# Performance work log

Measured on AMD Instinct MI355X. Metric: run time of the kernel, lower is better.

The kernel has to match this reference:

```python
import jax, jax.numpy as jnp
import numpy as np

N = 100000      # points
M = 12500       # cluster centers
E0 = 1600000    # point-level edges
E1 = 400000     # cluster-level edges
F_IN = 4        # raw point feature dim (e.g. intensity + extras)
D = 64          # hidden feature width
N_CLASSES = 8


def setup_inputs() -> dict:
    key = jax.random.key(0)
    ks = jax.random.split(key, 20)
    s = 0.05
    d = {}
    d["features"] = jax.random.normal(ks[0], (N, F_IN), jnp.float32)
    d["points"] = jax.random.normal(ks[1], (N, 3), jnp.float32)
    d["cluster_centers"] = jax.random.normal(ks[2], (M, 3), jnp.float32)
    d["l0_edges"] = jax.random.randint(ks[3], (E0, 2), 0, N)
    d["l1_edges"] = jax.random.randint(ks[4], (E1, 2), 0, M)
    d["labels"] = jax.random.randint(ks[5], (N,), 0, M)
    # Feature_extract MLP
    d["W_fe"] = s * jax.random.normal(ks[6], (F_IN + 3, D), jnp.float32)
    d["b_fe"] = jnp.zeros((D,), jnp.float32)
    # 4 Mini_GNN layers (layer2, layer2_1, layer6, layer6_1), stacked
    d["mini_We"] = s * jax.random.normal(ks[7], (4, D + 3, D), jnp.float32)
    d["mini_be"] = jnp.zeros((4, D), jnp.float32)
    d["mini_Wu"] = s * jax.random.normal(ks[8], (4, D, D), jnp.float32)
    d["mini_bu"] = jnp.zeros((4, D), jnp.float32)
    # Mini_to_Large
    d["W_m1"] = s * jax.random.normal(ks[9], (D + 3, D), jnp.float32)
    d["b_m1"] = jnp.zeros((D,), jnp.float32)
    d["W_m2"] = s * jax.random.normal(ks[10], (D, D), jnp.float32)
    d["b_m2"] = jnp.zeros((D,), jnp.float32)
    # 2 GNN layers on cluster graph (layer4, layer4_1), stacked
    d["gnn_We"] = s * jax.random.normal(ks[11], (2, D + 3, D), jnp.float32)
    d["gnn_be"] = jnp.zeros((2, D), jnp.float32)
    d["gnn_Wu"] = s * jax.random.normal(ks[12], (2, D, D), jnp.float32)
    d["gnn_bu"] = jnp.zeros((2, D), jnp.float32)
    # Large_to_Mini
    d["W_l"] = s * jax.random.normal(ks[13], (D + 3, D), jnp.float32)
    d["b_l"] = jnp.zeros((D,), jnp.float32)
    # Classifier
    d["W_c"] = s * jax.random.normal(ks[14], (D, N_CLASSES), jnp.float32)
    d["b_c"] = jnp.zeros((N_CLASSES,), jnp.float32)
    return d


def _gnn_layer(feat, pos, edges, We, be, Wu, bu, n_nodes):
    """PointGNN-style layer: gather -> edge MLP -> scatter max -> update MLP -> residual."""
    src, dst = edges[:, 0], edges[:, 1]
    e_in = jnp.concatenate([pos[src] - pos[dst], feat[src]], axis=-1)  # [E, 3+D]
    h = jax.nn.relu(e_in @ We + be)                                     # [E, D]
    agg = jax.ops.segment_max(h, dst, num_segments=n_nodes)            # [n, D]
    agg = jnp.where(jnp.isneginf(agg), 0.0, agg)  # nodes with no in-edges -> 0
    return jax.nn.relu(agg @ Wu + bu) + feat


def reference(features, points, cluster_centers, l0_edges, l1_edges, labels,
              W_fe, b_fe, mini_We, mini_be, mini_Wu, mini_bu,
              W_m1, b_m1, W_m2, b_m2, gnn_We, gnn_be, gnn_Wu, gnn_bu,
              W_l, b_l, W_c, b_c):
    rel = points - cluster_centers[labels]  # [N, 3] point pos relative to its cluster
    # layer1: Feature_extract
    f1 = jax.nn.relu(jnp.concatenate([features, rel], -1) @ W_fe + b_fe)
    # layer2 / layer2_1: Mini_GNN (scatter max) on point graph
    f2 = _gnn_layer(f1, points, l0_edges, mini_We[0], mini_be[0], mini_Wu[0], mini_bu[0], N)
    f2_1 = _gnn_layer(f2, points, l0_edges, mini_We[1], mini_be[1], mini_Wu[1], mini_bu[1], N)
    # layer3: Mini_to_Large (scatter sum by labels)
    h = jax.nn.relu(jnp.concatenate([f2_1, rel], -1) @ W_m1 + b_m1)
    c = jax.ops.segment_sum(h, labels, num_segments=M)  # [M, D]
    f3 = jax.nn.relu(c @ W_m2 + b_m2)
    # layer4 / layer4_1: GNN (scatter max) on cluster graph
    f4 = _gnn_layer(f3, cluster_centers, l1_edges, gnn_We[0], gnn_be[0], gnn_Wu[0], gnn_bu[0], M)
    f4_1 = _gnn_layer(f4, cluster_centers, l1_edges, gnn_We[1], gnn_be[1], gnn_Wu[1], gnn_bu[1], M)
    # layer5: Large_to_Mini (gather by labels)
    f5 = jax.nn.relu(jnp.concatenate([f4_1[labels], rel], -1) @ W_l + b_l)
    # layer6 / layer6_1 with residual skips per call()
    f6 = _gnn_layer(f5, points, l0_edges, mini_We[2], mini_be[2], mini_Wu[2], mini_bu[2], N)
    f6 = f6 + f2_1
    f6_1 = _gnn_layer(f6, points, l0_edges, mini_We[3], mini_be[3], mini_Wu[3], mini_bu[3], N)
    final = f6_1 + f2
    return final @ W_c + b_c  # [N, N_CLASSES] per-point logits
```

## Files before the change

### kernel.cpp

```cpp
#include <hip/hip_runtime.h>

#define N_PTS   100000
#define M_CL    12500
#define E0_N    1600000
#define E1_N    400000

#define NB      256
#define BIN_CAP 32
#define RANGE0  391
#define RANGE1  49
#define BCAP0   8192
#define BCAP1   2048
#define BCAPL   1024

#define LSTR    72

typedef unsigned short ushortT;
typedef short  short8 __attribute__((ext_vector_type(8)));
typedef float  v4f    __attribute__((ext_vector_type(4)));
typedef _Float16 h2   __attribute__((ext_vector_type(2)));
typedef unsigned u4v  __attribute__((ext_vector_type(4)));

__device__ inline ushortT f2bf(float x){
  union{float f; unsigned u;} v; v.f = x;
  unsigned r = v.u + 0x7fffu + ((v.u >> 16) & 1u);
  return (ushortT)(r >> 16);
}
__device__ inline float bf2f(ushortT h){
  union{unsigned u; float f;} v; v.u = ((unsigned)h) << 16;
  return v.f;
}
__device__ inline ushortT f2h(float x){
  union{_Float16 h; ushortT u;} v; v.h = (_Float16)x;
  return v.u;
}
__device__ inline float h2f(ushortT u){
  union{ushortT u; _Float16 h;} v; v.u = u;
  return (float)v.h;
}
__device__ inline h2 pkmax(h2 a, h2 b){ return __builtin_elementwise_max(a, b); }
__device__ inline h2 u2h(unsigned u){ union{unsigned u; h2 h;} v{u}; return v.h; }


struct WSrc { const float* p[16]; };

__global__ __launch_bounds__(256) void k_init_wprep(WSrc s, ushortT* __restrict__ wt, ushortT* __restrict__ wtc,
                                                    int* c0, int* c1, int* cL){
  int blk = blockIdx.x;
  if (blk == 0){
    int t = threadIdx.x;
    c0[t] = t*BCAP0; c1[t] = t*BCAP1; cL[t] = t*BCAPL;
    return;
  }
  int slot = blk - 1;
  if (slot < 15){
    const float* src = s.p[slot];
    ushortT* dst = wt + slot*4096;
    for (int e=threadIdx.x; e<4096; e+=256){
      int nn = e>>6, kk = e&63;
      dst[e] = f2bf(src[kk*64+nn]);
    }
  } else {
    const float* src = s.p[15];
    for (int e=threadIdx.x; e<1024; e+=256){
      int nn = e>>6, kk = e&63;
      wtc[e] = (nn<8) ? f2bf(src[kk*8+nn]) : (ushortT)0;
    }
  }
}


template<int RANGE, bool LAB>
__device__ void bin_seg(const int* __restrict__ edges, int E,
                        int* __restrict__ bcur, unsigned* __restrict__ tmp,
                        int bid, int nblk,
                        unsigned* stage, int* scnt, int* sbase){
  int tid = threadIdx.x;
  int nchunks = (E + 2047) / 2048;
  for (int c = bid; c < nchunks; c += nblk){
    int base = c*2048;
    scnt[tid] = 0;
    __syncthreads();
    #pragma unroll
    for (int r=0;r<8;++r){
      int e = base + r*256 + tid;
      if (e < E){
        int s, d;
        if (LAB){ s = e; d = edges[e]; }
        else    { s = edges[2*e]; d = edges[2*e+1]; }
        int bk = d / RANGE;
        unsigned packed = ((unsigned)s << 11) | (unsigned)(d - bk*RANGE);
        int pos = atomicAdd(&scnt[bk], 1);
        if (pos < BIN_CAP) stage[bk*BIN_CAP+pos] = packed;
        else tmp[atomicAdd(&bcur[bk],1)] = packed;
      }
    }
    __syncthreads();
    {
      int nfl = scnt[tid]; if (nfl > BIN_CAP) nfl = BIN_CAP;
      sbase[tid] = atomicAdd(&bcur[tid], nfl);
    }
    __syncthreads();
    int wv = tid >> 6, ln = tid & 63;
    for (int bb=0; bb<32; ++bb){
      int bk = wv*64 + bb*2 + (ln>>5);
      int ent = ln & 31;
      int nf = scnt[bk]; if (nf > BIN_CAP) nf = BIN_CAP;
      if (ent < nf) tmp[sbase[bk]+ent] = stage[bk*BIN_CAP+ent];
    }
    __syncthreads();
  }
}

__global__ __launch_bounds__(256) void k_bin_all(const int* __restrict__ l0e, const int* __restrict__ l1e,
                                                 const int* __restrict__ labels,
                                                 int* bc0, int* bc1, int* bcL,
                                                 unsigned* t0, unsigned* t1, unsigned* tL){
  __shared__ unsigned stage[NB*BIN_CAP];
  __shared__ int scnt[NB];
  __shared__ int sbase[NB];
  int b = blockIdx.x;
  if (b < 256)      bin_seg<RANGE0,false>(l0e, E0_N, bc0, t0, b, 256, stage, scnt, sbase);
  else if (b < 452) bin_seg<RANGE1,false>(l1e, E1_N, bc1, t1, b-256, 196, stage, scnt, sbase);
  else              bin_seg<RANGE1,true >(labels, N_PTS, bcL, tL, b-452, 49, stage, scnt, sbase);
}

__global__ void k_scan_all(const int* c0, int* bb0, int* e0,
                           const int* c1, int* bb1, int* e1,
                           const int* cL, int* bbL, int* eL){
  const int* cur; int* bb; int* offe; int BC;
  if (blockIdx.x == 0){ cur=c0; bb=bb0; offe=e0; BC=BCAP0; }
  else if (blockIdx.x == 1){ cur=c1; bb=bb1; offe=e1; BC=BCAP1; }
  else { cur=cL; bb=bbL; offe=eL; BC=BCAPL; }
  int lane = threadIdx.x & 63;
  int base = lane*4;
  int v0 = cur[base+0] - (base+0)*BC;
  int v1 = cur[base+1] - (base+1)*BC;
  int v2 = cur[base+2] - (base+2)*BC;
  int v3 = cur[base+3] - (base+3)*BC;
  int psum = v0+v1+v2+v3, sc = psum;
  #pragma unroll
  for (int st=1; st<64; st<<=1){
    int x = __shfl_up(sc, st, 64);
    if (lane >= st) sc += x;
  }
  int ex = sc - psum;
  bb[base+0] = ex;
  bb[base+1] = ex + v0;
  bb[base+2] = ex + v0 + v1;
  bb[base+3] = ex + v0 + v1 + v2;
  if (lane == 63) *offe = sc;
}

template<int RANGE, int BCAP, int K>
__device__ void csr_build_seg(const unsigned* __restrict__ tmp, const int* __restrict__ bcur,
                              const int* __restrict__ bb, int n,
                              int* __restrict__ offs, int* __restrict__ csr,
                              int b, int* hist, int* part){
  int tid = threadIdx.x;
  int dlo = b*RANGE;
  int range = n - dlo; if (range > RANGE) range = RANGE; if (range < 0) range = 0;
  int cnt = bcur[b] - b*BCAP;
  for (int t=tid; t<RANGE; t+=256) hist[t] = 0;
  __syncthreads();
  const unsigned* sl = tmp + (size_t)b*BCAP;
  for (int j=tid; j<cnt; j+=256) atomicAdd(&hist[sl[j] & 2047u], 1);
  __syncthreads();
  int s = 0; int loc[K];
  #pragma unroll
  for (int kk=0; kk<K; ++kk){
    int idx = tid*K + kk;
    int v = (idx < RANGE) ? hist[idx] : 0;
    loc[kk] = s; s += v;
  }
  part[tid] = s; __syncthreads();
  int own = s;
  for (int st=1; st<256; st<<=1){
    int x = (tid >= st) ? part[tid-st] : 0;
    __syncthreads();
    part[tid] += x;
    __syncthreads();
  }
  int ebase = part[tid] - own;
  int gb = bb[b];
  __syncthreads();
  #pragma unroll
  for (int kk=0; kk<K; ++kk){
    int idx = tid*K + kk;
    if (idx < RANGE){
      int ex = ebase + loc[kk];
      if (idx < range) offs[dlo+idx] = gb + ex;
      hist[idx] = ex;
    }
  }
  __syncthreads();
  for (int j=tid; j<cnt; j+=256){
    unsigned p = sl[j];
    int pos = atomicAdd(&hist[p & 2047u], 1);
    csr[gb + pos] = (int)(p >> 11);
  }
}

__global__ __launch_bounds__(256) void k_build_all(
    const unsigned* t0, const int* bc0, const int* bb0, int* offs0, int* csr0,
    const unsigned* t1, const int* bc1, const int* bb1, int* offs1, int* csr1,
    const unsigned* tL, const int* bcL, const int* bbL, int* offsL, int* csrL){
  __shared__ int hist[RANGE0];
  __shared__ int part[256];
  int b = blockIdx.x;
  if (b < 256)      csr_build_seg<RANGE0,BCAP0,2>(t0, bc0, bb0, N_PTS, offs0, csr0, b, hist, part);
  else if (b < 512) csr_build_seg<RANGE1,BCAP1,1>(t1, bc1, bb1, M_CL, offs1, csr1, b-256, hist, part);
  else              csr_build_seg<RANGE1,BCAPL,1>(tL, bcL, bbL, M_CL, offsL, csrL, b-512, hist, part);
}


__global__ __launch_bounds__(256) void k_f1g(const float* __restrict__ features, const float* __restrict__ points,
                                             const float* __restrict__ centers, const int* __restrict__ labels,
                                             const float* __restrict__ W, const float* __restrict__ b,
                                             const ushortT* __restrict__ Wt2, const float* __restrict__ bias2,
                                             const float* __restrict__ Wr2,
                                             float* __restrict__ rel, ushortT* __restrict__ f1b,
                                             ushortT* __restrict__ gout, int n, int ntiles){
  __shared__ ushortT lds[4*16*LSTR];
  int tid = threadIdx.x;
  int lane = tid & 63, wslot = tid >> 6;
  int quad = lane >> 4, l15 = lane & 15;
  int gw = (blockIdx.x*256 + tid) >> 6;
  int nw = (gridDim.x*256) >> 6;
  float Wf0=W[0*64+lane], Wf1=W[1*64+lane], Wf2=W[2*64+lane], Wf3=W[3*64+lane];
  float wr0=W[4*64+lane], wr1=W[5*64+lane], wr2=W[6*64+lane];
  float bias=b[lane];
  short8 s0_0 = *(const short8*)(Wt2 + ( 0 + l15)*64 +  0 + quad*8);
  short8 s0_1 = *(const short8*)(Wt2 + ( 0 + l15)*64 + 32 + quad*8);
  short8 s1_0 = *(const short8*)(Wt2 + (16 + l15)*64 +  0 + quad*8);
  short8 s1_1 = *(const short8*)(Wt2 + (16 + l15)*64 + 32 + quad*8);
  short8 s2_0 = *(const short8*)(Wt2 + (32 + l15)*64 +  0 + quad*8);
  short8 s2_1 = *(const short8*)(Wt2 + (32 + l15)*64 + 32 + quad*8);
  short8 s3_0 = *(const short8*)(Wt2 + (48 + l15)*64 +  0 + quad*8);
  short8 s3_1 = *(const short8*)(Wt2 + (48 + l15)*64 + 32 + quad*8);
  float eb0 = bias2[l15], eb1 = bias2[16+l15], eb2 = bias2[32+l15], eb3 = bias2[48+l15];
  float e0c0=Wr2[0*64+l15], e0c1=Wr2[0*64+16+l15], e0c2=Wr2[0*64+32+l15], e0c3=Wr2[0*64+48+l15];
  float e1c0=Wr2[1*64+l15], e1c1=Wr2[1*64+16+l15], e1c2=Wr2[1*64+32+l15], e1c3=Wr2[1*64+48+l15];
  float e2c0=Wr2[2*64+l15], e2c1=Wr2[2*64+16+l15], e2c2=Wr2[2*64+32+l15], e2c3=Wr2[2*64+48+l15];

  for (int t=gw; t<ntiles; t+=nw){
    int i0 = t*16;
    for (int r=0;r<16;++r){
      int row = i0 + r;
      bool ok = row < n;
      int rr = ok ? row : n-1;
      int lb = labels[rr];
      float rx = points[rr*3+0]-centers[lb*3+0];
      float ry = points[rr*3+1]-centers[lb*3+1];
      float rz = points[rr*3+2]-centers[lb*3+2];
      float acc = bias + wr0*rx + wr1*ry + wr2*rz;
      acc += features[rr*4+0]*Wf0 + features[rr*4+1]*Wf1;
      acc += features[rr*4+2]*Wf2 + features[rr*4+3]*Wf3;
      acc = fmaxf(acc, 0.f);
      ushortT ab = f2bf(acc);
      if (ok){
        f1b[(size_t)row*64+lane] = ab;
        if (lane==0){ rel[row*3+0]=rx; rel[row*3+1]=ry; rel[row*3+2]=rz; }
      }
      lds[wslot*(16*LSTR) + r*LSTR + lane] = ab;
    }
    __builtin_amdgcn_wave_barrier();
    const ushortT* lp = lds + wslot*(16*LSTR) + l15*LSTR + quad*8;
    short8 sa0 = *(const short8*)(lp);
    short8 sa1 = *(const short8*)(lp + 32);
    __builtin_amdgcn_wave_barrier();
    v4f ec0 = {0.f,0.f,0.f,0.f}, ec1 = ec0, ec2 = ec0, ec3 = ec0;
    ec0 = __builtin_amdgcn_mfma_f32_16x16x32_bf16(sa0, s0_0, ec0, 0,0,0);
    ec1 = __builtin_amdgcn_mfma_f32_16x16x32_bf16(sa0, s1_0, ec1, 0,0,0);
    ec2 = __builtin_amdgcn_mfma_f32_16x16x32_bf16(sa0, s2_0, ec2, 0,0,0);
    ec3 = __builtin_amdgcn_mfma_f32_16x16x32_bf16(sa0, s3_0, ec3, 0,0,0);
    ec0 = __builtin_amdgcn_mfma_f32_16x16x32_bf16(sa1, s0_1, ec0, 0,0,0);
    ec1 = __builtin_amdgcn_mfma_f32_16x16x32_bf16(sa1, s1_1, ec1, 0,0,0);
    ec2 = __builtin_amdgcn_mfma_f32_16x16x32_bf16(sa1, s2_1, ec2, 0,0,0);
    ec3 = __builtin_amdgcn_mfma_f32_16x16x32_bf16(sa1, s3_1, ec3, 0,0,0);
    #pragma unroll
    for (int r=0;r<4;++r){
      int row = i0 + quad*4 + r;
      if (row < n){
        float vx=points[row*3+0], vy=points[row*3+1], vz=points[row*3+2];
        float g0 = ec0[r] + eb0 + vx*e0c0 + vy*e1c0 + vz*e2c0;
        float g1 = ec1[r] + eb1 + vx*e0c1 + vy*e1c1 + vz*e2c1;
        float g2 = ec2[r] + eb2 + vx*e0c2 + vy*e1c2 + vz*e2c2;
        float g3 = ec3[r] + eb3 + vx*e0c3 + vy*e1c3 + vz*e2c3;
        size_t base = (size_t)row*64 + l15;
        gout[base] = f2h(g0); gout[base+16] = f2h(g1); gout[base+32] = f2h(g2); gout[base+48] = f2h(g3);
      }
    }
  }
}


template<bool RELU, int NRES, bool USEREL, bool GATHER, bool OUT16, bool F16O, int EMODE, bool ERELU>
__global__ __launch_bounds__(256) void k_gemm(
    const ushortT* __restrict__ A, const ushortT* __restrict__ Wt,
    const float* __restrict__ bias, const float* __restrict__ Wr,
    const float* __restrict__ rel, const int* __restrict__ gidx,
    const ushortT* __restrict__ r1, const ushortT* __restrict__ r2,
    ushortT* __restrict__ out16,
    const ushortT* __restrict__ Wt2, const float* __restrict__ bias2,
    const float* __restrict__ Wr2, const float* __restrict__ vec2,
    void* __restrict__ eout,
    int n, int ntiles)
{
  constexpr int LDSZ = (EMODE>0) ? 4*16*LSTR : 4;
  __shared__ ushortT lds[LDSZ];
  int tid = threadIdx.x;
  int lane = tid & 63, wslot = tid >> 6;
  int quad = lane >> 4, l15 = lane & 15;
  int gw = (blockIdx.x*256 + tid) >> 6;
  int nw = (gridDim.x*256) >> 6;

  short8 bfr0_0 = *(const short8*)(Wt + ( 0 + l15)*64 +  0 + quad*8);
  short8 bfr0_1 = *(const short8*)(Wt + ( 0 + l15)*64 + 32 + quad*8);
  short8 bfr1_0 = *(const short8*)(Wt + (16 + l15)*64 +  0 + quad*8);
  short8 bfr1_1 = *(const short8*)(Wt + (16 + l15)*64 + 32 + quad*8);
  short8 bfr2_0 = *(const short8*)(Wt + (32 + l15)*64 +  0 + quad*8);
  short8 bfr2_1 = *(const short8*)(Wt + (32 + l15)*64 + 32 + quad*8);
  short8 bfr3_0 = *(const short8*)(Wt + (48 + l15)*64 +  0 + quad*8);
  short8 bfr3_1 = *(const short8*)(Wt + (48 + l15)*64 + 32 + quad*8);
  float bs0 = bias[ 0 + l15], bs1 = bias[16 + l15];
  float bs2 = bias[32 + l15], bs3 = bias[48 + l15];
  float w0c0=0,w0c1=0,w0c2=0,w0c3=0, w1c0=0,w1c1=0,w1c2=0,w1c3=0, w2c0=0,w2c1=0,w2c2=0,w2c3=0;
  if (USEREL){
    w0c0=Wr[0*64+l15]; w0c1=Wr[0*64+16+l15]; w0c2=Wr[0*64+32+l15]; w0c3=Wr[0*64+48+l15];
    w1c0=Wr[1*64+l15]; w1c1=Wr[1*64+16+l15]; w1c2=Wr[1*64+32+l15]; w1c3=Wr[1*64+48+l15];
    w2c0=Wr[2*64+l15]; w2c1=Wr[2*64+16+l15]; w2c2=Wr[2*64+32+l15]; w2c3=Wr[2*64+48+l15];
  }

  short8 s0_0{}, s0_1{}, s1_0{}, s1_1{}, s2_0{}, s2_1{}, s3_0{}, s3_1{};
  float eb0=0, eb1=0, eb2=0, eb3=0;
  float e0c0=0,e0c1=0,e0c2=0,e0c3=0, e1c0=0,e1c1=0,e1c2=0,e1c3=0, e2c0=0,e2c1=0,e2c2=0,e2c3=0;
  float ebias_c = 0.f;
  if (EMODE == 1){
    s0_0 = *(const short8*)(Wt2 + ( 0 + l15)*64 +  0 + quad*8);
    s0_1 = *(const short8*)(Wt2 + ( 0 + l15)*64 + 32 + quad*8);
    s1_0 = *(const short8*)(Wt2 + (16 + l15)*64 +  0 + quad*8);
    s1_1 = *(const short8*)(Wt2 + (16 + l15)*64 + 32 + quad*8);
    s2_0 = *(const short8*)(Wt2 + (32 + l15)*64 +  0 + quad*8);
    s2_1 = *(const short8*)(Wt2 + (32 + l15)*64 + 32 + quad*8);
    s3_0 = *(const short8*)(Wt2 + (48 + l15)*64 +  0 + quad*8);
    s3_1 = *(const short8*)(Wt2 + (48 + l15)*64 + 32 + quad*8);
    eb0 = bias2[l15]; eb1 = bias2[16+l15]; eb2 = bias2[32+l15]; eb3 = bias2[48+l15];
    e0c0=Wr2[0*64+l15]; e0c1=Wr2[0*64+16+l15]; e0c2=Wr2[0*64+32+l15]; e0c3=Wr2[0*64+48+l15];
    e1c0=Wr2[1*64+l15]; e1c1=Wr2[1*64+16+l15]; e1c2=Wr2[1*64+32+l15]; e1c3=Wr2[1*64+48+l15];
    e2c0=Wr2[2*64+l15]; e2c1=Wr2[2*64+16+l15]; e2c2=Wr2[2*64+32+l15]; e2c3=Wr2[2*64+48+l15];
  } else if (EMODE == 2){
    s0_0 = *(const short8*)(Wt2 + l15*64 +  0 + quad*8);
    s0_1 = *(const short8*)(Wt2 + l15*64 + 32 + quad*8);
    ebias_c = (l15 < 8) ? bias2[l15] : 0.f;
  }

  for (int t=gw; t<ntiles; t+=nw){
    int i0 = t*16;
    int rowA = i0 + l15; if (rowA >= n) rowA = n-1;
    if (GATHER) rowA = gidx[rowA];
    const ushortT* ap = A + (size_t)rowA*64 + quad*8;
    short8 a0 = *(const short8*)(ap);
    short8 a1 = *(const short8*)(ap + 32);
    v4f ac0 = {0.f,0.f,0.f,0.f}, ac1 = ac0, ac2 = ac0, ac3 = ac0;
    ac0 = __builtin_amdgcn_mfma_f32_16x16x32_bf16(a0, bfr0_0, ac0, 0,0,0);
    ac1 = __builtin_amdgcn_mfma_f32_16x16x32_bf16(a0, bfr1_0, ac1, 0,0,0);
    ac2 = __builtin_amdgcn_mfma_f32_16x16x32_bf16(a0, bfr2_0, ac2, 0,0,0);
    ac3 = __builtin_amdgcn_mfma_f32_16x16x32_bf16(a0, bfr3_0, ac3, 0,0,0);
    ac0 = __builtin_amdgcn_mfma_f32_16x16x32_bf16(a1, bfr0_1, ac0, 0,0,0);
    ac1 = __builtin_amdgcn_mfma_f32_16x16x32_bf16(a1, bfr1_1, ac1, 0,0,0);
    ac2 = __builtin_amdgcn_mfma_f32_16x16x32_bf16(a1, bfr2_1, ac2, 0,0,0);
    ac3 = __builtin_amdgcn_mfma_f32_16x16x32_bf16(a1, bfr3_1, ac3, 0,0,0);

    #pragma unroll
    for (int r=0;r<4;++r){
      int row = i0 + quad*4 + r;
      bool rowok = (row < n);
      float rx=0.f, ry=0.f, rz=0.f;
      if (USEREL && rowok){ rx=rel[row*3+0]; ry=rel[row*3+1]; rz=rel[row*3+2]; }
      float v0 = ac0[r] + bs0, v1 = ac1[r] + bs1, v2 = ac2[r] + bs2, v3 = ac3[r] + bs3;
      if (USEREL){
        v0 += rx*w0c0 + ry*w1c0 + rz*w2c0;
        v1 += rx*w0c1 + ry*w1c1 + rz*w2c1;
        v2 += rx*w0c2 + ry*w1c2 + rz*w2c2;
        v3 += rx*w0c3 + ry*w1c3 + rz*w2c3;
      }
      if (RELU){ v0=fmaxf(v0,0.f); v1=fmaxf(v1,0.f); v2=fmaxf(v2,0.f); v3=fmaxf(v3,0.f); }
      size_t base = (size_t)row*64 + l15;
      if (rowok){
        if (NRES>=1){
          v0 += bf2f(r1[base]); v1 += bf2f(r1[base+16]); v2 += bf2f(r1[base+32]); v3 += bf2f(r1[base+48]);
        }
        if (NRES>=2){
          v0 += bf2f(r2[base]); v1 += bf2f(r2[base+16]); v2 += bf2f(r2[base+32]); v3 += bf2f(r2[base+48]);
        }
        if (OUT16){
          if (F16O){
            out16[base] = f2h(v0); out16[base+16] = f2h(v1); out16[base+32] = f2h(v2); out16[base+48] = f2h(v3);
          } else {
            out16[base] = f2bf(v0); out16[base+16] = f2bf(v1); out16[base+32] = f2bf(v2); out16[base+48] = f2bf(v3);
          }
        }
      }
      if (EMODE > 0){
        int lb = wslot*(16*LSTR) + (quad*4+r)*LSTR + l15;
        lds[lb]      = f2bf(v0);
        lds[lb + 16] = f2bf(v1);
        lds[lb + 32] = f2bf(v2);
        lds[lb + 48] = f2bf(v3);
      }
    }

    if (EMODE > 0){
      __builtin_amdgcn_wave_barrier();
      const ushortT* lp = lds + wslot*(16*LSTR) + l15*LSTR + quad*8;
      short8 sa0 = *(const short8*)(lp);
      short8 sa1 = *(const short8*)(lp + 32);
      __builtin_amdgcn_wave_barrier();
      if (EMODE == 1){
        v4f ec0 = {0.f,0.f,0.f,0.f}, ec1 = ec0, ec2 = ec0, ec3 = ec0;
        ec0 = __builtin_amdgcn_mfma_f32_16x16x32_bf16(sa0, s0_0, ec0, 0,0,0);
        ec1 = __builtin_amdgcn_mfma_f32_16x16x32_bf16(sa0, s1_0, ec1, 0,0,0);
        ec2 = __builtin_amdgcn_mfma_f32_16x16x32_bf16(sa0, s2_0, ec2, 0,0,0);
        ec3 = __builtin_amdgcn_mfma_f32_16x16x32_bf16(sa0, s3_0, ec3, 0,0,0);
        ec0 = __builtin_amdgcn_mfma_f32_16x16x32_bf16(sa1, s0_1, ec0, 0,0,0);
        ec1 = __builtin_amdgcn_mfma_f32_16x16x32_bf16(sa1, s1_1, ec1, 0,0,0);
        ec2 = __builtin_amdgcn_mfma_f32_16x16x32_bf16(sa1, s2_1, ec2, 0,0,0);
        ec3 = __builtin_amdgcn_mfma_f32_16x16x32_bf16(sa1, s3_1, ec3, 0,0,0);
        ushortT* eo = (ushortT*)eout;
        #pragma unroll
        for (int r=0;r<4;++r){
          int row = i0 + quad*4 + r;
          if (row < n){
            float vx=vec2[row*3+0], vy=vec2[row*3+1], vz=vec2[row*3+2];
            float g0 = ec0[r] + eb0 + vx*e0c0 + vy*e1c0 + vz*e2c0;
            float g1 = ec1[r] + eb1 + vx*e0c1 + vy*e1c1 + vz*e2c1;
            float g2 = ec2[r] + eb2 + vx*e0c2 + vy*e1c2 + vz*e2c2;
            float g3 = ec3[r] + eb3 + vx*e0c3 + vy*e1c3 + vz*e2c3;
            if (ERELU){ g0=fmaxf(g0,0.f); g1=fmaxf(g1,0.f); g2=fmaxf(g2,0.f); g3=fmaxf(g3,0.f); }
            size_t base = (size_t)row*64 + l15;
            eo[base] = f2h(g0); eo[base+16] = f2h(g1); eo[base+32] = f2h(g2); eo[base+48] = f2h(g3);
          }
        }
      } else {
        v4f ec = {0.f,0.f,0.f,0.f};
        ec = __builtin_amdgcn_mfma_f32_16x16x32_bf16(sa0, s0_0, ec, 0,0,0);
        ec = __builtin_amdgcn_mfma_f32_16x16x32_bf16(sa1, s0_1, ec, 0,0,0);
        if (l15 < 8){
          float* eo = (float*)eout;
          #pragma unroll
          for (int r=0;r<4;++r){
            int row = i0 + quad*4 + r;
            if (row < n) eo[(size_t)row*8 + l15] = ec[r] + ebias_c;
          }
        }
      }
    }
  }
}


__global__ __launch_bounds__(256) void k_edge_agg(const int* __restrict__ offs, const int* __restrict__ csr,
                                                  const float* __restrict__ pos, const ushortT* __restrict__ g,
                                                  const float* __restrict__ Wp, ushortT* __restrict__ agg, int n){
  int lane = threadIdx.x & 63;
  int grp = lane >> 3, d8 = lane & 7;
  int gbase = lane & 56;
  int gw = (blockIdx.x*256 + threadIdx.x) >> 6;
  int nw = (gridDim.x*256) >> 6;
  const u4v* g4 = (const u4v*)g;
  float2 w0[4], w1[4], w2[4];
  #pragma unroll
  for (int q=0;q<4;++q){
    w0[q] = *(const float2*)(Wp + 0*64 + d8*8 + 2*q);
    w1[q] = *(const float2*)(Wp + 1*64 + d8*8 + 2*q);
    w2[q] = *(const float2*)(Wp + 2*64 + d8*8 + 2*q);
  }
  const h2 NEGBIG = {(_Float16)-60000.f, (_Float16)-60000.f};
  int n8 = (n+7) >> 3;
  for (int ii=gw; ii<n8; ii+=nw){
    int i0 = ii*8;
    int ig = i0 + grp; bool ok = ig < n; if (!ok) ig = n-1;
    int b = offs[ig], e = offs[ig+1];
    int cnt = e - b, c1 = cnt - 1;
    int mx = cnt;
    mx = max(mx, __shfl_xor(mx, 8, 64));
    mx = max(mx, __shfl_xor(mx, 16, 64));
    mx = max(mx, __shfl_xor(mx, 32, 64));
    h2 m0=NEGBIG, m1=NEGBIG, m2=NEGBIG, m3=NEGBIG;
    for (int J=0; J<mx; J+=8){
      if (J < cnt){
        int sv = csr[b + min(J + d8, c1)];
        #pragma unroll
        for (int jj=0; jj<8; ++jj){
          int s = __shfl(sv, gbase + jj, 64);
          u4v u = g4[(size_t)s*8 + d8];
          m0 = pkmax(m0, u2h(u.x));
          m1 = pkmax(m1, u2h(u.y));
          m2 = pkmax(m2, u2h(u.z));
          m3 = pkmax(m3, u2h(u.w));
        }
      }
    }
    float px = pos[ig*3+0], py = pos[ig*3+1], pz = pos[ig*3+2];
    u4v outv;
    {
      float sA = w0[0].x*px + w1[0].x*py + w2[0].x*pz;
      float sB = w0[0].y*px + w1[0].y*py + w2[0].y*pz;
      outv.x = (unsigned)f2bf(fmaxf((float)m0.x - sA, 0.f)) |
               ((unsigned)f2bf(fmaxf((float)m0.y - sB, 0.f)) << 16);
    }
    {
      float sA = w0[1].x*px + w1[1].x*py + w2[1].x*pz;
      float sB = w0[1].y*px + w1[1].y*py + w2[1].y*pz;
      outv.y = (unsigned)f2bf(fmaxf((float)m1.x - sA, 0.f)) |
               ((unsigned)f2bf(fmaxf((float)m1.y - sB, 0.f)) << 16);
    }
    {
      float sA = w0[2].x*px + w1[2].x*py + w2[2].x*pz;
      float sB = w0[2].y*px + w1[2].y*py + w2[2].y*pz;
      outv.z = (unsigned)f2bf(fmaxf((float)m2.x - sA, 0.f)) |
               ((unsigned)f2bf(fmaxf((float)m2.y - sB, 0.f)) << 16);
    }
    {
      float sA = w0[3].x*px + w1[3].x*py + w2[3].x*pz;
      float sB = w0[3].y*px + w1[3].y*py + w2[3].y*pz;
      outv.w = (unsigned)f2bf(fmaxf((float)m3.x - sA, 0.f)) |
               ((unsigned)f2bf(fmaxf((float)m3.y - sB, 0.f)) << 16);
    }
    if (ok) ((u4v*)agg)[(size_t)ig*8 + d8] = outv;
  }
}


__global__ __launch_bounds__(256) void k_seg_gather(const int* __restrict__ offs, const int* __restrict__ csr,
                                                    const ushortT* __restrict__ h, ushortT* __restrict__ c, int m){
  int lane = threadIdx.x & 63;
  int wv = (blockIdx.x*256 + threadIdx.x) >> 6;
  if (wv >= m) return;
  int b = offs[wv], e = offs[wv+1];
  float acc = 0.f;
  for (int k=b; k<e; ++k){
    int i = csr[k];
    acc += h2f(h[(size_t)i*64+lane]);
  }
  c[(size_t)wv*64+lane] = f2bf(acc);
}


extern "C" void kernel_launch(void* const* d_in, const int* in_sizes, int n_in,
                              void* d_out, int out_size, void* d_ws, size_t ws_size,
                              hipStream_t stream){
  const float* features = (const float*)d_in[0];
  const float* points   = (const float*)d_in[1];
  const float* centers  = (const float*)d_in[2];
  const int*   l0e      = (const int*)d_in[3];
  const int*   l1e      = (const int*)d_in[4];
  const int*   labels   = (const int*)d_in[5];
  const float* W_fe = (const float*)d_in[6];
  const float* b_fe = (const float*)d_in[7];
  const float* mWe  = (const float*)d_in[8];
  const float* mbe  = (const float*)d_in[9];
  const float* mWu  = (const float*)d_in[10];
  const float* mbu  = (const float*)d_in[11];
  const float* W_m1 = (const float*)d_in[12];
  const float* b_m1 = (const float*)d_in[13];
  const float* W_m2 = (const float*)d_in[14];
  const float* b_m2 = (const float*)d_in[15];
  const float* gWe  = (const float*)d_in[16];
  const float* gbe  = (const float*)d_in[17];
  const float* gWu  = (const float*)d_in[18];
  const float* gbu  = (const float*)d_in[19];
  const float* W_l  = (const float*)d_in[20];
  const float* b_l  = (const float*)d_in[21];
  const float* W_c  = (const float*)d_in[22];
  const float* b_c  = (const float*)d_in[23];
  float* out = (float*)d_out;

  char* w = (char*)d_ws;
  size_t off = 0;
  auto alloc = [&](size_t bytes)->void*{
    void* p = (void*)(w + off);
    off = (off + bytes + 255) & ~(size_t)255;
    return p;
  };
  float* rel  = (float*)alloc((size_t)N_PTS*3*4);
  ushortT* UF1 = (ushortT*)alloc((size_t)N_PTS*64*2);
  ushortT* UF2 = (ushortT*)alloc((size_t)N_PTS*64*2);
  ushortT* UF21= (ushortT*)alloc((size_t)N_PTS*64*2);
  ushortT* UF5 = (ushortT*)alloc((size_t)N_PTS*64*2);
  ushortT* UF6 = (ushortT*)alloc((size_t)N_PTS*64*2);
  ushortT* gbuf= (ushortT*)alloc((size_t)N_PTS*64*2);
  ushortT* abuf= (ushortT*)alloc((size_t)N_PTS*64*2);
  ushortT* cb_b= (ushortT*)alloc((size_t)M_CL*64*2);
  ushortT* UF3 = (ushortT*)alloc((size_t)M_CL*64*2);
  ushortT* UF4 = (ushortT*)alloc((size_t)M_CL*64*2);
  ushortT* cg_b= (ushortT*)alloc((size_t)M_CL*64*2);
  ushortT* cagg_b = (ushortT*)alloc((size_t)M_CL*64*2);
  ushortT* f41_b  = (ushortT*)alloc((size_t)M_CL*64*2);
  ushortT* wt  = (ushortT*)alloc((size_t)15*4096*2);
  ushortT* wtc = (ushortT*)alloc((size_t)1024*2);
  int* offs0 = (int*)alloc((size_t)(N_PTS+1)*4);
  int* csr0  = (int*)alloc((size_t)E0_N*4);
  int* offs1 = (int*)alloc((size_t)(M_CL+1)*4);
  int* csr1  = (int*)alloc((size_t)E1_N*4);
  int* offsL = (int*)alloc((size_t)(M_CL+1)*4);
  int* csrL  = (int*)alloc((size_t)N_PTS*4);
  unsigned* tmp0 = (unsigned*)alloc((size_t)NB*BCAP0*4);
  unsigned* tmp1 = (unsigned*)alloc((size_t)NB*BCAP1*4);
  unsigned* tmpL = (unsigned*)alloc((size_t)NB*BCAPL*4);
  int* bcur0 = (int*)alloc(NB*4);
  int* bcur1 = (int*)alloc(NB*4);
  int* bcurL = (int*)alloc(NB*4);
  int* bb0   = (int*)alloc(NB*4);
  int* bb1   = (int*)alloc(NB*4);
  int* bbL   = (int*)alloc(NB*4);
  (void)ws_size; (void)in_sizes; (void)n_in; (void)out_size;

  const int NT_N = (N_PTS+15)/16;
  const int NT_M = (M_CL +15)/16;
  const int GBG_N = 1563;
  const int GBG_M = 196;
  const int GB_N  = 3125;

  WSrc ws{};
  ws.p[0]=mWu+0*4096; ws.p[1]=mWu+1*4096; ws.p[2]=mWu+2*4096; ws.p[3]=mWu+3*4096;
  ws.p[4]=W_m2; ws.p[5]=gWu+0*4096; ws.p[6]=gWu+1*4096;
  ws.p[7]=mWe+0*4288+192; ws.p[8]=mWe+1*4288+192; ws.p[9]=mWe+2*4288+192; ws.p[10]=mWe+3*4288+192;
  ws.p[11]=W_m1; ws.p[12]=W_l; ws.p[13]=gWe+0*4288+192; ws.p[14]=gWe+1*4288+192;
  ws.p[15]=W_c;
  k_init_wprep<<<17, 256, 0, stream>>>(ws, wt, wtc, bcur0, bcur1, bcurL);
  k_bin_all<<<501, 256, 0, stream>>>(l0e, l1e, labels, bcur0, bcur1, bcurL, tmp0, tmp1, tmpL);
  k_scan_all<<<3, 64, 0, stream>>>(bcur0, bb0, offs0+N_PTS, bcur1, bb1, offs1+M_CL, bcurL, bbL, offsL+M_CL);
  k_build_all<<<768, 256, 0, stream>>>(tmp0, bcur0, bb0, offs0, csr0,
                                       tmp1, bcur1, bb1, offs1, csr1,
                                       tmpL, bcurL, bbL, offsL, csrL);

  k_f1g<<<GBG_N, 256, 0, stream>>>(features, points, centers, labels, W_fe, b_fe,
      wt+7*4096, mbe+0, mWe+0*4288, rel, UF1, gbuf, N_PTS, NT_N);

  k_edge_agg<<<GB_N,256,0,stream>>>(offs0, csr0, points, gbuf, mWe+0*4288, abuf, N_PTS);
  k_gemm<true,1,false,false,true,false,1,false><<<GBG_N,256,0,stream>>>(abuf, wt+0*4096, mbu+0,
      nullptr, nullptr, nullptr, UF1, nullptr, UF2,
      wt+8*4096, mbe+64, mWe+1*4288, points, gbuf, N_PTS, NT_N);
  k_edge_agg<<<GB_N,256,0,stream>>>(offs0, csr0, points, gbuf, mWe+1*4288, abuf, N_PTS);
  k_gemm<true,1,false,false,true,false,1,true><<<GBG_N,256,0,stream>>>(abuf, wt+1*4096, mbu+64,
      nullptr, nullptr, nullptr, UF2, nullptr, UF21,
      wt+11*4096, b_m1, W_m1+4096, rel, gbuf, N_PTS, NT_N);
  k_seg_gather<<<(M_CL*64+255)/256, 256, 0, stream>>>(offsL, csrL, gbuf, cb_b, M_CL);
  k_gemm<true,0,false,false,true,false,1,false><<<GBG_M,256,0,stream>>>(cb_b, wt+4*4096, b_m2,
      nullptr, nullptr, nullptr, nullptr, nullptr, UF3,
      wt+13*4096, gbe+0, gWe+0*4288, centers, cg_b, M_CL, NT_M);
  k_edge_agg<<<GBG_M,256,0,stream>>>(offs1, csr1, centers, cg_b, gWe+0*4288, cagg_b, M_CL);
  k_gemm<true,1,false,false,true,false,1,false><<<GBG_M,256,0,stream>>>(cagg_b, wt+5*4096, gbu+0,
      nullptr, nullptr, nullptr, UF3, nullptr, UF4,
      wt+14*4096, gbe+64, gWe+1*4288, centers, cg_b, M_CL, NT_M);
  k_edge_agg<<<GBG_M,256,0,stream>>>(offs1, csr1, centers, cg_b, gWe+1*4288, cagg_b, M_CL);
  k_gemm<true,1,false,false,true,false,0,false><<<GBG_M,256,0,stream>>>(cagg_b, wt+6*4096, gbu+64,
      nullptr, nullptr, nullptr, UF4, nullptr, f41_b,
      nullptr, nullptr, nullptr, nullptr, nullptr, M_CL, NT_M);
  k_gemm<true,0,true,true,true,false,1,false><<<GBG_N,256,0,stream>>>(f41_b, wt+12*4096, b_l,
      W_l+4096, rel, labels, nullptr, nullptr, UF5,
      wt+9*4096, mbe+128, mWe+2*4288, points, gbuf, N_PTS, NT_N);
  k_edge_agg<<<GB_N,256,0,stream>>>(offs0, csr0, points, gbuf, mWe+2*4288, abuf, N_PTS);
  k_gemm<true,2,false,false,true,false,1,false><<<GBG_N,256,0,stream>>>(abuf, wt+2*4096, mbu+128,
      nullptr, nullptr, nullptr, UF5, UF21, UF6,
      wt+10*4096, mbe+192, mWe+3*4288, points, gbuf, N_PTS, NT_N);
  k_edge_agg<<<GB_N,256,0,stream>>>(offs0, csr0, points, gbuf, mWe+3*4288, abuf, N_PTS);
  k_gemm<true,2,false,false,false,false,2,false><<<GBG_N,256,0,stream>>>(abuf, wt+3*4096, mbu+192,
      nullptr, nullptr, nullptr, UF6, UF2, nullptr,
      wtc, b_c, nullptr, nullptr, out, N_PTS, NT_N);
}
```

Before: 479.6 us.

## Permute feature column layout for vectorized stores and merge binning with f1 kernel

Result: faster. 460.3 us (-4.0%).

```diff
diff --git a/kernel.cpp b/kernel.cpp
--- a/kernel.cpp
+++ b/kernel.cpp
@@ -1,4 +1,5 @@
 #include <hip/hip_runtime.h>
+
 
 #define N_PTS   100000
 #define M_CL    12500
@@ -17,6 +18,7 @@
 
 typedef unsigned short ushortT;
 typedef short  short8 __attribute__((ext_vector_type(8)));
+typedef short  s4v    __attribute__((ext_vector_type(4)));
 typedef float  v4f    __attribute__((ext_vector_type(4)));
 typedef _Float16 h2   __attribute__((ext_vector_type(2)));
 typedef unsigned u4v  __attribute__((ext_vector_type(4)));
@@ -42,9 +44,10 @@
 __device__ inline h2 u2h(unsigned u){ union{unsigned u; h2 h;} v{u}; return v.h; }
 
 
-struct WSrc { const float* p[16]; };
+struct WSrc { const float* p[22]; };
 
 __global__ __launch_bounds__(256) void k_init_wprep(WSrc s, ushortT* __restrict__ wt, ushortT* __restrict__ wtc,
+                                                    float* __restrict__ wpp,
                                                     int* c0, int* c1, int* cL){
   int blk = blockIdx.x;
   if (blk == 0){
@@ -57,14 +60,21 @@
     const float* src = s.p[slot];
     ushortT* dst = wt + slot*4096;
     for (int e=threadIdx.x; e<4096; e+=256){
-      int nn = e>>6, kk = e&63;
+      int nn = e>>6, p = e&63;
+      int kk = (p&3)*16 + (p>>2);
       dst[e] = f2bf(src[kk*64+nn]);
     }
-  } else {
+  } else if (slot == 15){
     const float* src = s.p[15];
     for (int e=threadIdx.x; e<1024; e+=256){
-      int nn = e>>6, kk = e&63;
+      int nn = e>>6, p = e&63;
+      int kk = (p&3)*16 + (p>>2);
       wtc[e] = (nn<8) ? f2bf(src[kk*8+nn]) : (ushortT)0;
+    }
+  } else {
+    for (int e=threadIdx.x; e<6*192; e+=256){
+      int i = e/192, rem = e - i*192, r = rem>>6, p = rem&63;
+      wpp[e] = s.p[16+i][r*64 + ((p&3)*16 + (p>>2))];
     }
   }
 }
@@ -112,19 +122,6 @@
   }
 }
 
-__global__ __launch_bounds__(256) void k_bin_all(const int* __restrict__ l0e, const int* __restrict__ l1e,
-                                                 const int* __restrict__ labels,
-                                                 int* bc0, int* bc1, int* bcL,
-                                                 unsigned* t0, unsigned* t1, unsigned* tL){
-  __shared__ unsigned stage[NB*BIN_CAP];
-  __shared__ int scnt[NB];
-  __shared__ int sbase[NB];
-  int b = blockIdx.x;
-  if (b < 256)      bin_seg<RANGE0,false>(l0e, E0_N, bc0, t0, b, 256, stage, scnt, sbase);
-  else if (b < 452) bin_seg<RANGE1,false>(l1e, E1_N, bc1, t1, b-256, 196, stage, scnt, sbase);
-  else              bin_seg<RANGE1,true >(labels, N_PTS, bcL, tL, b-452, 49, stage, scnt, sbase);
-}
-
 __global__ void k_scan_all(const int* c0, int* bb0, int* e0,
                            const int* c1, int* bb1, int* e1,
                            const int* cL, int* bbL, int* eL){
@@ -214,22 +211,40 @@
 }
 
 
-__global__ __launch_bounds__(256) void k_f1g(const float* __restrict__ features, const float* __restrict__ points,
-                                             const float* __restrict__ centers, const int* __restrict__ labels,
-                                             const float* __restrict__ W, const float* __restrict__ b,
-                                             const ushortT* __restrict__ Wt2, const float* __restrict__ bias2,
-                                             const float* __restrict__ Wr2,
-                                             float* __restrict__ rel, ushortT* __restrict__ f1b,
-                                             ushortT* __restrict__ gout, int n, int ntiles){
-  __shared__ ushortT lds[4*16*LSTR];
+__global__ __launch_bounds__(256) void k_bin_f1g(
+    const int* __restrict__ l0e, const int* __restrict__ l1e, const int* __restrict__ labels,
+    int* bc0, int* bc1, int* bcL,
+    unsigned* t0, unsigned* t1, unsigned* tL,
+    const float* __restrict__ features, const float* __restrict__ points,
+    const float* __restrict__ centers,
+    const float* __restrict__ W, const float* __restrict__ bfe,
+    const ushortT* __restrict__ Wt2, const float* __restrict__ bias2,
+    const float* __restrict__ Wr2,
+    float* __restrict__ rel, ushortT* __restrict__ f1b,
+    ushortT* __restrict__ gout, int n, int ntiles, int nf1blk)
+{
+  __shared__ char smem[34816];
+  int b = blockIdx.x;
+  if (b < 501){
+    unsigned* stage = (unsigned*)smem;
+    int* scnt = (int*)(smem + 32768);
+    int* sbase = (int*)(smem + 33792);
+    if (b < 256)      bin_seg<RANGE0,false>(l0e, E0_N, bc0, t0, b, 256, stage, scnt, sbase);
+    else if (b < 452) bin_seg<RANGE1,false>(l1e, E1_N, bc1, t1, b-256, 196, stage, scnt, sbase);
+    else              bin_seg<RANGE1,true >(labels, N_PTS, bcL, tL, b-452, 49, stage, scnt, sbase);
+    return;
+  }
+  ushortT* lds = (ushortT*)smem;
+  int bb = b - 501;
   int tid = threadIdx.x;
   int lane = tid & 63, wslot = tid >> 6;
   int quad = lane >> 4, l15 = lane & 15;
-  int gw = (blockIdx.x*256 + tid) >> 6;
-  int nw = (gridDim.x*256) >> 6;
+  int permL = (lane & 15)*4 + (lane >> 4);
+  int gw = (bb*256 + tid) >> 6;
+  int nw = (nf1blk*256) >> 6;
   float Wf0=W[0*64+lane], Wf1=W[1*64+lane], Wf2=W[2*64+lane], Wf3=W[3*64+lane];
   float wr0=W[4*64+lane], wr1=W[5*64+lane], wr2=W[6*64+lane];
-  float bias=b[lane];
+  float bias=bfe[lane];
   short8 s0_0 = *(const short8*)(Wt2 + ( 0 + l15)*64 +  0 + quad*8);
   short8 s0_1 = *(const short8*)(Wt2 + ( 0 + l15)*64 + 32 + quad*8);
   short8 s1_0 = *(const short8*)(Wt2 + (16 + l15)*64 +  0 + quad*8);
@@ -259,10 +274,10 @@
       acc = fmaxf(acc, 0.f);
       ushortT ab = f2bf(acc);
       if (ok){
-        f1b[(size_t)row*64+lane] = ab;
+        f1b[(size_t)row*64 + permL] = ab;
         if (lane==0){ rel[row*3+0]=rx; rel[row*3+1]=ry; rel[row*3+2]=rz; }
       }
-      lds[wslot*(16*LSTR) + r*LSTR + lane] = ab;
+      lds[wslot*(16*LSTR) + r*LSTR + permL] = ab;
     }
     __builtin_amdgcn_wave_barrier();
     const ushortT* lp = lds + wslot*(16*LSTR) + l15*LSTR + quad*8;
@@ -287,8 +302,8 @@
         float g1 = ec1[r] + eb1 + vx*e0c1 + vy*e1c1 + vz*e2c1;
         float g2 = ec2[r] + eb2 + vx*e0c2 + vy*e1c2 + vz*e2c2;
         float g3 = ec3[r] + eb3 + vx*e0c3 + vy*e1c3 + vz*e2c3;
-        size_t base = (size_t)row*64 + l15;
-        gout[base] = f2h(g0); gout[base+16] = f2h(g1); gout[base+32] = f2h(g2); gout[base+48] = f2h(g3);
+        s4v o; o.x=(short)f2h(g0); o.y=(short)f2h(g1); o.z=(short)f2h(g2); o.w=(short)f2h(g3);
+        *(s4v*)(gout + (size_t)row*64 + l15*4) = o;
       }
     }
   }
@@ -386,28 +401,29 @@
         v3 += rx*w0c3 + ry*w1c3 + rz*w2c3;
       }
       if (RELU){ v0=fmaxf(v0,0.f); v1=fmaxf(v1,0.f); v2=fmaxf(v2,0.f); v3=fmaxf(v3,0.f); }
-      size_t base = (size_t)row*64 + l15;
+      size_t pb = (size_t)row*64 + l15*4;
       if (rowok){
         if (NRES>=1){
-          v0 += bf2f(r1[base]); v1 += bf2f(r1[base+16]); v2 += bf2f(r1[base+32]); v3 += bf2f(r1[base+48]);
+          s4v rv = *(const s4v*)(r1 + pb);
+          v0 += bf2f((ushortT)rv.x); v1 += bf2f((ushortT)rv.y);
+          v2 += bf2f((ushortT)rv.z); v3 += bf2f((ushortT)rv.w);
         }
         if (NRES>=2){
-          v0 += bf2f(r2[base]); v1 += bf2f(r2[base+16]); v2 += bf2f(r2[base+32]); v3 += bf2f(r2[base+48]);
+          s4v rv = *(const s4v*)(r2 + pb);
+          v0 += bf2f((ushortT)rv.x); v1 += bf2f((ushortT)rv.y);
+          v2 += bf2f((ushortT)rv.z); v3 += bf2f((ushortT)rv.w);
         }
         if (OUT16){
-          if (F16O){
-            out16[base] = f2h(v0); out16[base+16] = f2h(v1); out16[base+32] = f2h(v2); out16[base+48] = f2h(v3);
-          } else {
-            out16[base] = f2bf(v0); out16[base+16] = f2bf(v1); out16[base+32] = f2bf(v2); out16[base+48] = f2bf(v3);
-          }
+          s4v o;
+          if (F16O){ o.x=(short)f2h(v0); o.y=(short)f2h(v1); o.z=(short)f2h(v2); o.w=(short)f2h(v3); }
+          else     { o.x=(short)f2bf(v0); o.y=(short)f2bf(v1); o.z=(short)f2bf(v2); o.w=(short)f2bf(v3); }
+          *(s4v*)(out16 + pb) = o;
         }
       }
       if (EMODE > 0){
-        int lb = wslot*(16*LSTR) + (quad*4+r)*LSTR + l15;
-        lds[lb]      = f2bf(v0);
-        lds[lb + 16] = f2bf(v1);
-        lds[lb + 32] = f2bf(v2);
-        lds[lb + 48] = f2bf(v3);
+        int lb = wslot*(16*LSTR) + (quad*4+r)*LSTR + l15*4;
+        s4v o; o.x=(short)f2bf(v0); o.y=(short)f2bf(v1); o.z=(short)f2bf(v2); o.w=(short)f2bf(v3);
+        *(s4v*)(lds + lb) = o;
       }
     }
 
@@ -438,8 +454,8 @@
             float g2 = ec2[r] + eb2 + vx*e0c2 + vy*e1c2 + vz*e2c2;
             float g3 = ec3[r] + eb3 + vx*e0c3 + vy*e1c3 + vz*e2c3;
             if (ERELU){ g0=fmaxf(g0,0.f); g1=fmaxf(g1,0.f); g2=fmaxf(g2,0.f); g3=fmaxf(g3,0.f); }
-            size_t base = (size_t)row*64 + l15;
-            eo[base] = f2h(g0); eo[base+16] = f2h(g1); eo[base+32] = f2h(g2); eo[base+48] = f2h(g3);
+            s4v o; o.x=(short)f2h(g0); o.y=(short)f2h(g1); o.z=(short)f2h(g2); o.w=(short)f2h(g3);
+            *(s4v*)(eo + (size_t)row*64 + l15*4) = o;
           }
         }
       } else {
@@ -600,6 +616,7 @@
   ushortT* f41_b  = (ushortT*)alloc((size_t)M_CL*64*2);
   ushortT* wt  = (ushortT*)alloc((size_t)15*4096*2);
   ushortT* wtc = (ushortT*)alloc((size_t)1024*2);
+  float* wpp = (float*)alloc((size_t)6*192*4);
   int* offs0 = (int*)alloc((size_t)(N_PTS+1)*4);
   int* csr0  = (int*)alloc((size_t)E0_N*4);
   int* offs1 = (int*)alloc((size_t)(M_CL+1)*4);
@@ -629,21 +646,22 @@
   ws.p[7]=mWe+0*4288+192; ws.p[8]=mWe+1*4288+192; ws.p[9]=mWe+2*4288+192; ws.p[10]=mWe+3*4288+192;
   ws.p[11]=W_m1; ws.p[12]=W_l; ws.p[13]=gWe+0*4288+192; ws.p[14]=gWe+1*4288+192;
   ws.p[15]=W_c;
-  k_init_wprep<<<17, 256, 0, stream>>>(ws, wt, wtc, bcur0, bcur1, bcurL);
-  k_bin_all<<<501, 256, 0, stream>>>(l0e, l1e, labels, bcur0, bcur1, bcurL, tmp0, tmp1, tmpL);
+  ws.p[16]=mWe+0*4288; ws.p[17]=mWe+1*4288; ws.p[18]=mWe+2*4288; ws.p[19]=mWe+3*4288;
+  ws.p[20]=gWe+0*4288; ws.p[21]=gWe+1*4288;
+  k_init_wprep<<<18, 256, 0, stream>>>(ws, wt, wtc, wpp, bcur0, bcur1, bcurL);
+  k_bin_f1g<<<501 + GBG_N, 256, 0, stream>>>(l0e, l1e, labels, bcur0, bcur1, bcurL, tmp0, tmp1, tmpL,
+      features, points, centers, W_fe, b_fe,
+      wt+7*4096, mbe+0, mWe+0*4288, rel, UF1, gbuf, N_PTS, NT_N, GBG_N);
   k_scan_all<<<3, 64, 0, stream>>>(bcur0, bb0, offs0+N_PTS, bcur1, bb1, offs1+M_CL, bcurL, bbL, offsL+M_CL);
   k_build_all<<<768, 256, 0, stream>>>(tmp0, bcur0, bb0, offs0, csr0,
                                        tmp1, bcur1, bb1, offs1, csr1,
                                        tmpL, bcurL, bbL, offsL, csrL);
 
-  k_f1g<<<GBG_N, 256, 0, stream>>>(features, points, centers, labels, W_fe, b_fe,
-      wt+7*4096, mbe+0, mWe+0*4288, rel, UF1, gbuf, N_PTS, NT_N);
-
-  k_edge_agg<<<GB_N,256,0,stream>>>(offs0, csr0, points, gbuf, mWe+0*4288, abuf, N_PTS);
+  k_edge_agg<<<GB_N,256,0,stream>>>(offs0, csr0, points, gbuf, wpp+0*192, abuf, N_PTS);
   k_gemm<true,1,false,false,true,false,1,false><<<GBG_N,256,0,stream>>>(abuf, wt+0*4096, mbu+0,
       nullptr, nullptr, nullptr, UF1, nullptr, UF2,
       wt+8*4096, mbe+64, mWe+1*4288, points, gbuf, N_PTS, NT_N);
-  k_edge_agg<<<GB_N,256,0,stream>>>(offs0, csr0, points, gbuf, mWe+1*4288, abuf, N_PTS);
+  k_edge_agg<<<GB_N,256,0,stream>>>(offs0, csr0, points, gbuf, wpp+1*192, abuf, N_PTS);
   k_gemm<true,1,false,false,true,false,1,true><<<GBG_N,256,0,stream>>>(abuf, wt+1*4096, mbu+64,
       nullptr, nullptr, nullptr, UF2, nullptr, UF21,
       wt+11*4096, b_m1, W_m1+4096, rel, gbuf, N_PTS, NT_N);
@@ -651,22 +669,22 @@
   k_gemm<true,0,false,false,true,false,1,false><<<GBG_M,256,0,stream>>>(cb_b, wt+4*4096, b_m2,
       nullptr, nullptr, nullptr, nullptr, nullptr, UF3,
       wt+13*4096, gbe+0, gWe+0*4288, centers, cg_b, M_CL, NT_M);
-  k_edge_agg<<<GBG_M,256,0,stream>>>(offs1, csr1, centers, cg_b, gWe+0*4288, cagg_b, M_CL);
+  k_edge_agg<<<GBG_M,256,0,stream>>>(offs1, csr1, centers, cg_b, wpp+4*192, cagg_b, M_CL);
   k_gemm<true,1,false,false,true,false,1,false><<<GBG_M,256,0,stream>>>(cagg_b, wt+5*4096, gbu+0,
       nullptr, nullptr, nullptr, UF3, nullptr, UF4,
       wt+14*4096, gbe+64, gWe+1*4288, centers, cg_b, M_CL, NT_M);
-  k_edge_agg<<<GBG_M,256,0,stream>>>(offs1, csr1, centers, cg_b, gWe+1*4288, cagg_b, M_CL);
+  k_edge_agg<<<GBG_M,256,0,stream>>>(offs1, csr1, centers, cg_b, wpp+5*192, cagg_b, M_CL);
   k_gemm<true,1,false,false,true,false,0,false><<<GBG_M,256,0,stream>>>(cagg_b, wt+6*4096, gbu+64,
       nullptr, nullptr, nullptr, UF4, nullptr, f41_b,
       nullptr, nullptr, nullptr, nullptr, nullptr, M_CL, NT_M);
   k_gemm<true,0,true,true,true,false,1,false><<<GBG_N,256,0,stream>>>(f41_b, wt+12*4096, b_l,
       W_l+4096, rel, labels, nullptr, nullptr, UF5,
       wt+9*4096, mbe+128, mWe+2*4288, points, gbuf, N_PTS, NT_N);
-  k_edge_agg<<<GB_N,256,0,stream>>>(offs0, csr0, points, gbuf, mWe+2*4288, abuf, N_PTS);
+  k_edge_agg<<<GB_N,256,0,stream>>>(offs0, csr0, points, gbuf, wpp+2*192, abuf, N_PTS);
   k_gemm<true,2,false,false,true,false,1,false><<<GBG_N,256,0,stream>>>(abuf, wt+2*4096, mbu+128,
       nullptr, nullptr, nullptr, UF5, UF21, UF6,
       wt+10*4096, mbe+192, mWe+3*4288, points, gbuf, N_PTS, NT_N);
-  k_edge_agg<<<GB_N,256,0,stream>>>(offs0, csr0, points, gbuf, mWe+3*4288, abuf, N_PTS);
+  k_edge_agg<<<GB_N,256,0,stream>>>(offs0, csr0, points, gbuf, wpp+3*192, abuf, N_PTS);
   k_gemm<true,2,false,false,false,false,2,false><<<GBG_N,256,0,stream>>>(abuf, wt+3*4096, mbu+192,
       nullptr, nullptr, nullptr, UF6, UF2, nullptr,
       wtc, b_c, nullptr, nullptr, out, N_PTS, NT_N);
```
